# Optimization experiments

Hardware: AMD Instinct MI355X
Metric: run time of the kernel (lower is better)

The kernel has to match this reference:

```python
import jax, jax.numpy as jnp
import numpy as np

N = 8192       # patients (nodes)
E = 262144     # edges per graph (avg degree 32)
DF = 128       # dim_final
SLOPE = 0.25   # leaky_relu negative slope


def _spmm(rows, cols, vals, dense):
    # out[i] = sum_{e: rows[e]==i} vals[e] * dense[cols[e]]  == sparse_adj @ dense
    return jax.ops.segment_sum(vals[:, None] * dense[cols], rows, num_segments=N)


def _branch(x, rows, cols, vals, w1, b1, w2, b2):
    # GraphGCN: gc1 -> leaky_relu -> (dropout: identity in eval) -> gc2 -> leaky_relu
    h = _spmm(rows, cols, vals, x @ w1) + b1
    h = jax.nn.leaky_relu(h, negative_slope=SLOPE)
    h = _spmm(rows, cols, vals, h @ w2) + b2
    return jax.nn.leaky_relu(h, negative_slope=SLOPE)


def setup_inputs() -> dict:
    key = jax.random.key(0)
    ks = jax.random.split(key, 40)
    i = 0

    def xav(k, shape):
        std = (2.0 / (shape[0] + shape[1])) ** 0.5
        return std * jax.random.normal(k, shape, dtype=jnp.float32)

    inp = {}
    feat_dims = {"RNAseq": 4096, "dnam": 4096, "cn": 4096, "mic": 1024}
    for name, d in feat_dims.items():
        inp[name] = jax.random.normal(ks[i], (N, d), dtype=jnp.float32); i += 1
    for g in range(1, 5):
        inp[f"rows{g}"] = jax.random.randint(ks[i], (E,), 0, N, dtype=jnp.int32); i += 1
        inp[f"cols{g}"] = jax.random.randint(ks[i], (E,), 0, N, dtype=jnp.int32); i += 1
        inp[f"vals{g}"] = jax.random.uniform(ks[i], (E,), dtype=jnp.float32); i += 1
    # per-branch params: (in_dim, hid_dim); suffixes r=RNAseq, d=meth, c=CN, m=miRNA
    specs = {"r": (4096, 512), "d": (4096, 512), "c": (4096, 512), "m": (1024, 256)}
    for s, (din, dh) in specs.items():
        inp[f"w1_{s}"] = xav(ks[i], (din, dh)); i += 1
        inp[f"b1_{s}"] = jnp.zeros((dh,), jnp.float32)
        inp[f"w2_{s}"] = xav(ks[i], (dh, DF)); i += 1
        inp[f"b2_{s}"] = jnp.zeros((DF,), jnp.float32)
    return inp


def reference(RNAseq, dnam, cn, mic,
              rows1, cols1, vals1, rows2, cols2, vals2,
              rows3, cols3, vals3, rows4, cols4, vals4,
              w1_r, b1_r, w2_r, b2_r,
              w1_d, b1_d, w2_d, b2_d,
              w1_c, b1_c, w2_c, b2_c,
              w1_m, b1_m, w2_m, b2_m):
    x_r = _branch(RNAseq, rows1, cols1, vals1, w1_r, b1_r, w2_r, b2_r)
    x_d = _branch(dnam,   rows2, cols2, vals2, w1_d, b1_d, w2_d, b2_d)
    x_c = _branch(cn,     rows3, cols3, vals3, w1_c, b1_c, w2_c, b2_c)
    x_m = _branch(mic,    rows4, cols4, vals4, w1_m, b1_m, w2_m, b2_m)
    return (x_r + x_d + x_c + x_m) / 4.0
```

## Files before the change

kernel.cpp:

```cpp
#include <hip/hip_runtime.h>

#define N_NODES 8192
#define N_EDGES 262144
#define SLOPE 0.25f

typedef __attribute__((ext_vector_type(8))) short bf16x8;
typedef __attribute__((ext_vector_type(4))) float f32x4;

__device__ __forceinline__ float lrelu(float x) { return x >= 0.f ? x : SLOPE * x; }

__device__ __forceinline__ unsigned short bf16_rne(float x) {
    unsigned u = __float_as_uint(x);
    return (unsigned short)((u + 0x7FFFu + ((u >> 16) & 1u)) >> 16);
}
__device__ __forceinline__ float bf2f(unsigned short h) {
    return __uint_as_float(((unsigned)h) << 16);
}

#define GLDS16(g, l)                                                              \
    __builtin_amdgcn_global_load_lds((const __attribute__((address_space(1))) void*)(g), \
                                     (__attribute__((address_space(3))) void*)(l), 16, 0, 0)

struct RoundB { const float* src[4]; unsigned short* dst[4]; long long n4[4]; };

__global__ __launch_bounds__(256) void round_bf16(RoundB rb) {
    const int z = blockIdx.y;
    const long long i = (long long)blockIdx.x * 256 + threadIdx.x;
    if (i >= rb.n4[z]) return;
    const float4 a = reinterpret_cast<const float4*>(rb.src[z])[i];
    ushort4 h = {bf16_rne(a.x), bf16_rne(a.y), bf16_rne(a.z), bf16_rne(a.w)};
    reinterpret_cast<ushort4*>(rb.dst[z])[i] = h;
}

struct TransB { const float* W[4]; unsigned short* Th[4]; int K[4]; int N[4]; };

__global__ __launch_bounds__(256) void tsplit(TransB tb) {
    const int z = blockIdx.z;
    const int K = tb.K[z], N = tb.N[z];
    const int k0 = blockIdx.x * 32, n0 = blockIdx.y * 32;
    if (k0 >= K || n0 >= N) return;
    __shared__ float t[32][33];
    const int tx = threadIdx.x & 31, ty = threadIdx.x >> 5;
    const float* W = tb.W[z];
#pragma unroll
    for (int i = 0; i < 32; i += 8)
        t[ty + i][tx] = W[(size_t)(k0 + ty + i) * N + n0 + tx];
    __syncthreads();
#pragma unroll
    for (int i = 0; i < 32; i += 8) {
        const int n = ty + i;
        tb.Th[z][(size_t)(n0 + n) * K + k0 + tx] = bf16_rne(t[tx][n]);
    }
}

struct GemmB {
    const unsigned short* A[4];
    const unsigned short* Bh[4];
    unsigned short* C[4];
    int K[4];
    int NT[4];
};

template <int NF>
__global__ __launch_bounds__(256, 2) void gemm_bf16s(GemmB gb) {
    constexpr int BN = NF * 32;
    constexpr int BROWS = BN;
    constexpr int BGR_PER_THREAD = NF / 2;
    const int nwg = gridDim.x * gridDim.y * gridDim.z;
    int id = (blockIdx.z * gridDim.y + blockIdx.y) * gridDim.x + blockIdx.x;
    const int cpx = nwg >> 3;
    id = (id & 7) * cpx + (id >> 3);
    const int by = id % gridDim.y;
    const int rest = id / gridDim.y;
    const int bx = rest % gridDim.x;
    const int z = rest / gridDim.x;

    const int nt = gb.NT[z];
    if (by >= nt) return;
    const int K = gb.K[z];
    const int N = nt * BN;
    const unsigned short* __restrict__ A = gb.A[z];
    const unsigned short* __restrict__ Bh = gb.Bh[z];
    unsigned short* __restrict__ C = gb.C[z];

    __shared__ unsigned short As[3 * 128 * 32];
    __shared__ unsigned short Bs[3 * BROWS * 32];
    const int tid = threadIdx.x;
    const int w = tid >> 6, lane = tid & 63;
    const int wm = w >> 1, wn = w & 1;
    const int bm0 = bx * 128, bn0 = by * BN;

    auto stage = [&](int buf, int kt) {
        const int k0 = kt << 5;
#pragma unroll
        for (int i = 0; i < 2; ++i) {
            const int f = (w * 2 + i) * 64 + lane;
            const int row = f >> 2, s = f & 3;
            const int kg = s ^ ((row >> 1) & 3);
            GLDS16(A + (size_t)(bm0 + row) * K + k0 + kg * 8,
                   &As[buf * 4096 + (w * 2 + i) * 512]);
        }
#pragma unroll
        for (int i = 0; i < BGR_PER_THREAD; ++i) {
            const int f = (w * BGR_PER_THREAD + i) * 64 + lane;
            const int row = f >> 2, s = f & 3;
            const int kg = s ^ ((row >> 1) & 3);
            GLDS16(Bh + (size_t)(bn0 + row) * K + k0 + kg * 8,
                   &Bs[buf * (BROWS * 32) + (w * BGR_PER_THREAD + i) * 512]);
        }
    };

    f32x4 acc[4][NF];
#pragma unroll
    for (int mf = 0; mf < 4; ++mf)
#pragma unroll
        for (int nf = 0; nf < NF; ++nf) acc[mf][nf] = (f32x4){0.f, 0.f, 0.f, 0.f};

    const int nk = K >> 5;
    stage(0, 0);
    stage(1, 1);

    int c0 = 0, c1 = 1, c2 = 2;
    for (int t = 0; t < nk; ++t) {
        if (t + 2 < nk) {
            stage(c2, t + 2);
            if constexpr (NF == 8)
                asm volatile("s_waitcnt vmcnt(12)" ::: "memory");
            else
                asm volatile("s_waitcnt vmcnt(8)" ::: "memory");
        } else if (t + 1 < nk) {
            if constexpr (NF == 8)
                asm volatile("s_waitcnt vmcnt(6)" ::: "memory");
            else
                asm volatile("s_waitcnt vmcnt(4)" ::: "memory");
        } else {
            asm volatile("s_waitcnt vmcnt(0)" ::: "memory");
        }
        __builtin_amdgcn_s_barrier();
        __builtin_amdgcn_sched_barrier(0);

        const int kq = lane >> 4;
        bf16x8 a[4], b[NF];
#pragma unroll
        for (int mf = 0; mf < 4; ++mf) {
            const int r = wm * 64 + mf * 16 + (lane & 15);
            a[mf] = *reinterpret_cast<const bf16x8*>(
                &As[c0 * 4096 + r * 32 + ((kq ^ ((r >> 1) & 3)) << 3)]);
        }
#pragma unroll
        for (int nf = 0; nf < NF; ++nf) {
            const int r = wn * (NF * 16) + nf * 16 + (lane & 15);
            b[nf] = *reinterpret_cast<const bf16x8*>(
                &Bs[c0 * (BROWS * 32) + r * 32 + ((kq ^ ((r >> 1) & 3)) << 3)]);
        }
        __builtin_amdgcn_s_setprio(1);
#pragma unroll
        for (int mf = 0; mf < 4; ++mf)
#pragma unroll
            for (int nf = 0; nf < NF; ++nf)
                acc[mf][nf] = __builtin_amdgcn_mfma_f32_16x16x32_bf16(a[mf], b[nf], acc[mf][nf], 0, 0, 0);
        __builtin_amdgcn_s_setprio(0);

        __builtin_amdgcn_s_barrier();
        const int tmp = c0; c0 = c1; c1 = c2; c2 = tmp;
    }

    const int cr = (lane >> 4) * 4, cc = lane & 15;
#pragma unroll
    for (int mf = 0; mf < 4; ++mf)
#pragma unroll
        for (int nf = 0; nf < NF; ++nf)
#pragma unroll
            for (int j = 0; j < 4; ++j)
                C[(size_t)(bm0 + wm * 64 + mf * 16 + cr + j) * N + bn0 + wn * (NF * 16) + nf * 16 + cc] =
                    bf16_rne(acc[mf][nf][j]);
}

struct GraphPtrs {
    const int* r[4];
    const int* c[4];
    const float* v[4];
};

__global__ __launch_bounds__(256) void hist4(GraphPtrs p, int* __restrict__ cnt4) {
    const int g = blockIdx.y;
    const int e = blockIdx.x * 256 + threadIdx.x;
    atomicAdd(&cnt4[g * N_NODES + p.r[g][e]], 1);
}

__global__ __launch_bounds__(256) void scan4(const int* __restrict__ cnt4,
                                             int* __restrict__ rs4,
                                             int* __restrict__ cur4) {
    const int g = blockIdx.x;
    const int* cnt = cnt4 + g * N_NODES;
    int* row_start = rs4 + (size_t)g * (N_NODES + 1);
    int* cursor = cur4 + g * N_NODES;
    __shared__ int ssum[256];
    const int t = threadIdx.x;
    int local[32];
    int s = 0;
#pragma unroll
    for (int j = 0; j < 32; ++j) { local[j] = cnt[t * 32 + j]; s += local[j]; }
    ssum[t] = s;
    __syncthreads();
    for (int off = 1; off < 256; off <<= 1) {
        const int v = ssum[t];
        const int add = (t >= off) ? ssum[t - off] : 0;
        __syncthreads();
        ssum[t] = v + add;
        __syncthreads();
    }
    int run = (t == 0) ? 0 : ssum[t - 1];
#pragma unroll
    for (int j = 0; j < 32; ++j) {
        row_start[t * 32 + j] = run;
        cursor[t * 32 + j] = run;
        run += local[j];
    }
    if (t == 255) row_start[N_NODES] = run;
}

__global__ __launch_bounds__(256) void scatter4(GraphPtrs p, int* __restrict__ cur4,
                                                int* __restrict__ pcol4,
                                                float* __restrict__ pval4) {
    const int g = blockIdx.y;
    const int e = blockIdx.x * 256 + threadIdx.x;
    const int r = p.r[g][e];
    const int pos = atomicAdd(&cur4[g * N_NODES + r], 1);
    pcol4[(size_t)g * N_EDGES + pos] = p.c[g][e];
    pval4[(size_t)g * N_EDGES + pos] = p.v[g][e];
}

struct SpmmB {
    const int* rs[4];
    const int* pc[4];
    const float* pv[4];
    const unsigned short* Y[4];
    const float* bi[4];
    unsigned short* H[4];
};

template <int NC>
__global__ __launch_bounds__(256) void spmm_h1(SpmmB sb) {
    constexpr int PL = NC / 64;
    const int z = blockIdx.y;
    const int row = (blockIdx.x * 256 + threadIdx.x) >> 6;
    const int lane = threadIdx.x & 63;
    const int* rs = sb.rs[z];
    const int s = rs[row], e1 = rs[row + 1];
    const int* pc = sb.pc[z];
    const float* pv = sb.pv[z];
    const unsigned short* Y = sb.Y[z];
    const int base = lane * PL;

    float acc[PL];
#pragma unroll
    for (int j = 0; j < PL; ++j) acc[j] = 0.f;
    for (int e = s; e < e1; ++e) {
        const int c = pc[e];
        const float v = pv[e];
        const unsigned short* y = Y + (size_t)c * NC + base;
        if constexpr (PL == 8) {
            const bf16x8 raw = *reinterpret_cast<const bf16x8*>(y);
#pragma unroll
            for (int j = 0; j < 8; ++j)
                acc[j] = fmaf(v, bf2f((unsigned short)raw[j]), acc[j]);
        } else {
            const ushort4 raw = *reinterpret_cast<const ushort4*>(y);
            acc[0] = fmaf(v, bf2f(raw.x), acc[0]);
            acc[1] = fmaf(v, bf2f(raw.y), acc[1]);
            acc[2] = fmaf(v, bf2f(raw.z), acc[2]);
            acc[3] = fmaf(v, bf2f(raw.w), acc[3]);
        }
    }
    const float* bi = sb.bi[z];
    unsigned short* H = sb.H[z] + (size_t)row * NC + base;
    if constexpr (PL == 8) {
        bf16x8 vh;
#pragma unroll
        for (int j = 0; j < 8; ++j) vh[j] = (short)bf16_rne(lrelu(acc[j] + bi[base + j]));
        *reinterpret_cast<bf16x8*>(H) = vh;
    } else {
        ushort4 vh;
        vh.x = bf16_rne(lrelu(acc[0] + bi[base + 0]));
        vh.y = bf16_rne(lrelu(acc[1] + bi[base + 1]));
        vh.z = bf16_rne(lrelu(acc[2] + bi[base + 2]));
        vh.w = bf16_rne(lrelu(acc[3] + bi[base + 3]));
        *reinterpret_cast<ushort4*>(H) = vh;
    }
}

struct Out4 { const float* b2[4]; };

__global__ __launch_bounds__(256) void spmm_out4(const int* __restrict__ rs4,
                                                 const int* __restrict__ pc4,
                                                 const float* __restrict__ pv4,
                                                 const unsigned short* __restrict__ Y2all,
                                                 Out4 ob, float* __restrict__ out) {
    const int row = (blockIdx.x * 256 + threadIdx.x) >> 6;
    const int lane = threadIdx.x & 63;
    const int base = lane * 2;
    float r0 = 0.f, r1 = 0.f;
#pragma unroll
    for (int b = 0; b < 4; ++b) {
        const int* rs = rs4 + (size_t)b * (N_NODES + 1);
        const int s = rs[row], e1 = rs[row + 1];
        const int* pc = pc4 + (size_t)b * N_EDGES;
        const float* pv = pv4 + (size_t)b * N_EDGES;
        const unsigned short* Y = Y2all + (size_t)b * N_NODES * 128;
        float a0 = 0.f, a1 = 0.f;
        for (int e = s; e < e1; ++e) {
            const float v = pv[e];
            const unsigned u = *reinterpret_cast<const unsigned*>(Y + (size_t)pc[e] * 128 + base);
            a0 = fmaf(v, __uint_as_float(u << 16), a0);
            a1 = fmaf(v, __uint_as_float(u & 0xFFFF0000u), a1);
        }
        const float* bi = ob.b2[b];
        r0 += lrelu(a0 + bi[base]);
        r1 += lrelu(a1 + bi[base + 1]);
    }
    *reinterpret_cast<float2*>(out + (size_t)row * 128 + base) =
        make_float2(0.25f * r0, 0.25f * r1);
}

__global__ __launch_bounds__(256) void spmm_out1(const int* __restrict__ rs,
                                                 const int* __restrict__ pc,
                                                 const float* __restrict__ pv,
                                                 const unsigned short* __restrict__ Y,
                                                 const float* __restrict__ bias,
                                                 float* __restrict__ out, int first) {
    const int row = (blockIdx.x * 256 + threadIdx.x) >> 6;
    const int lane = threadIdx.x & 63;
    const int base = lane * 2;
    const int s = rs[row], e1 = rs[row + 1];
    float a0 = 0.f, a1 = 0.f;
    for (int e = s; e < e1; ++e) {
        const float v = pv[e];
        const unsigned u = *reinterpret_cast<const unsigned*>(Y + (size_t)pc[e] * 128 + base);
        a0 = fmaf(v, __uint_as_float(u << 16), a0);
        a1 = fmaf(v, __uint_as_float(u & 0xFFFF0000u), a1);
    }
    float r0 = 0.25f * lrelu(a0 + bias[base]);
    float r1 = 0.25f * lrelu(a1 + bias[base + 1]);
    float* o = out + (size_t)row * 128 + base;
    if (!first) {
        const float2 p = *reinterpret_cast<const float2*>(o);
        r0 += p.x;
        r1 += p.y;
    }
    *reinterpret_cast<float2*>(o) = make_float2(r0, r1);
}

extern "C" void kernel_launch(void* const* d_in, const int* in_sizes, int n_in,
                              void* d_out, int out_size, void* d_ws, size_t ws_size,
                              hipStream_t stream) {
    const float* X[4] = {(const float*)d_in[0], (const float*)d_in[1],
                         (const float*)d_in[2], (const float*)d_in[3]};
    GraphPtrs gp;
    for (int b = 0; b < 4; ++b) {
        gp.r[b] = (const int*)d_in[4 + 3 * b];
        gp.c[b] = (const int*)d_in[5 + 3 * b];
        gp.v[b] = (const float*)d_in[6 + 3 * b];
    }
    const float *w1[4], *b1[4], *w2[4], *b2[4];
    for (int b = 0; b < 4; ++b) {
        w1[b] = (const float*)d_in[16 + 4 * b + 0];
        b1[b] = (const float*)d_in[16 + 4 * b + 1];
        w2[b] = (const float*)d_in[16 + 4 * b + 2];
        b2[b] = (const float*)d_in[16 + 4 * b + 3];
    }
    const int din[4] = {4096, 4096, 4096, 1024};
    const int dh[4] = {512, 512, 512, 256};
    float* out = (float*)d_out;

    char* wsc = (char*)d_ws;
    size_t off = 0;
    auto carve = [&](size_t bytes) {
        void* p = wsc + off;
        off += (bytes + 255) & ~(size_t)255;
        return p;
    };
    int* cnt4 = (int*)carve((size_t)4 * N_NODES * 4);
    int* rs4 = (int*)carve((size_t)4 * (N_NODES + 1) * 4);
    int* cur4 = (int*)carve((size_t)4 * N_NODES * 4);
    int* pcol4 = (int*)carve((size_t)4 * N_EDGES * 4);
    float* pval4 = (float*)carve((size_t)4 * N_EDGES * 4);

    size_t tier1_base = off;
    unsigned short *Xbf[4], *W1h[4], *W2h[4], *Y1[4], *H1[4];
    for (int b = 0; b < 4; ++b) Xbf[b] = (unsigned short*)carve((size_t)N_NODES * din[b] * 2);
    for (int b = 0; b < 4; ++b) W1h[b] = (unsigned short*)carve((size_t)dh[b] * din[b] * 2);
    for (int b = 0; b < 4; ++b) W2h[b] = (unsigned short*)carve((size_t)128 * dh[b] * 2);
    for (int b = 0; b < 4; ++b) Y1[b] = (unsigned short*)carve((size_t)N_NODES * dh[b] * 2);
    for (int b = 0; b < 4; ++b) H1[b] = (unsigned short*)carve((size_t)N_NODES * dh[b] * 2);
    unsigned short* Y2all = (unsigned short*)carve((size_t)4 * N_NODES * 128 * 2);
    const bool tier1 = (off <= ws_size);
    unsigned short* Y2s[4];
    if (tier1) {
        for (int b = 0; b < 4; ++b) Y2s[b] = Y2all + (size_t)b * N_NODES * 128;
    } else {
        off = tier1_base;
        unsigned short* xb = (unsigned short*)carve((size_t)N_NODES * 4096 * 2);
        unsigned short* w1h = (unsigned short*)carve((size_t)512 * 4096 * 2);
        unsigned short* w2h = (unsigned short*)carve((size_t)128 * 512 * 2);
        unsigned short* y1 = (unsigned short*)carve((size_t)N_NODES * 512 * 2);
        unsigned short* h1 = (unsigned short*)carve((size_t)N_NODES * 512 * 2);
        unsigned short* y2 = (unsigned short*)carve((size_t)N_NODES * 128 * 2);
        for (int b = 0; b < 4; ++b) {
            Xbf[b] = xb; W1h[b] = w1h; W2h[b] = w2h;
            Y1[b] = y1; H1[b] = h1; Y2s[b] = y2;
        }
    }

    hipMemsetAsync(cnt4, 0, (size_t)4 * N_NODES * sizeof(int), stream);
    {
        dim3 g(N_EDGES / 256, 4);
        hist4<<<g, 256, 0, stream>>>(gp, cnt4);
        scan4<<<4, 256, 0, stream>>>(cnt4, rs4, cur4);
        scatter4<<<g, 256, 0, stream>>>(gp, cur4, pcol4, pval4);
    }

    if (tier1) {
        RoundB rb;
        for (int b = 0; b < 4; ++b) {
            rb.src[b] = X[b];
            rb.dst[b] = Xbf[b];
            rb.n4[b] = (long long)N_NODES * din[b] / 4;
        }
        round_bf16<<<dim3(32768, 4), 256, 0, stream>>>(rb);

        TransB t1;
        for (int b = 0; b < 4; ++b) {
            t1.W[b] = w1[b]; t1.Th[b] = W1h[b];
            t1.K[b] = din[b]; t1.N[b] = dh[b];
        }
        tsplit<<<dim3(128, 16, 4), 256, 0, stream>>>(t1);

        GemmB g1;
        for (int b = 0; b < 4; ++b) {
            g1.A[b] = Xbf[b]; g1.Bh[b] = W1h[b];
            g1.C[b] = Y1[b]; g1.K[b] = din[b]; g1.NT[b] = dh[b] / 256;
        }
        gemm_bf16s<8><<<dim3(64, 2, 4), 256, 0, stream>>>(g1);

        SpmmB s1;
        for (int b = 0; b < 4; ++b) {
            s1.rs[b] = rs4 + (size_t)b * (N_NODES + 1);
            s1.pc[b] = pcol4 + (size_t)b * N_EDGES;
            s1.pv[b] = pval4 + (size_t)b * N_EDGES;
            s1.Y[b] = Y1[b]; s1.bi[b] = b1[b]; s1.H[b] = H1[b];
        }
        spmm_h1<512><<<dim3(N_NODES / 4, 3), 256, 0, stream>>>(s1);
        SpmmB s1m = s1;
        s1m.rs[0] = s1.rs[3]; s1m.pc[0] = s1.pc[3]; s1m.pv[0] = s1.pv[3];
        s1m.Y[0] = s1.Y[3]; s1m.bi[0] = s1.bi[3]; s1m.H[0] = s1.H[3];
        spmm_h1<256><<<dim3(N_NODES / 4, 1), 256, 0, stream>>>(s1m);

        TransB t2;
        for (int b = 0; b < 4; ++b) {
            t2.W[b] = w2[b]; t2.Th[b] = W2h[b];
            t2.K[b] = dh[b]; t2.N[b] = 128;
        }
        tsplit<<<dim3(16, 4, 4), 256, 0, stream>>>(t2);

        GemmB g2;
        for (int b = 0; b < 4; ++b) {
            g2.A[b] = H1[b]; g2.Bh[b] = W2h[b];
            g2.C[b] = Y2s[b]; g2.K[b] = dh[b]; g2.NT[b] = 1;
        }
        gemm_bf16s<4><<<dim3(64, 1, 4), 256, 0, stream>>>(g2);

        Out4 ob;
        for (int b = 0; b < 4; ++b) ob.b2[b] = b2[b];
        spmm_out4<<<N_NODES / 4, 256, 0, stream>>>(rs4, pcol4, pval4, Y2all, ob, out);
    } else {
        for (int b = 0; b < 4; ++b) {
            RoundB rb;
            rb.src[0] = X[b]; rb.dst[0] = Xbf[b];
            rb.n4[0] = (long long)N_NODES * din[b] / 4;
            round_bf16<<<dim3((unsigned)(rb.n4[0] / 256), 1), 256, 0, stream>>>(rb);
            TransB t1;
            t1.W[0] = w1[b]; t1.Th[0] = W1h[b];
            t1.K[0] = din[b]; t1.N[0] = dh[b];
            tsplit<<<dim3(din[b] / 32, dh[b] / 32, 1), 256, 0, stream>>>(t1);
            GemmB g1;
            g1.A[0] = Xbf[b]; g1.Bh[0] = W1h[b];
            g1.C[0] = Y1[b]; g1.K[0] = din[b]; g1.NT[0] = dh[b] / 256;
            gemm_bf16s<8><<<dim3(64, dh[b] / 256, 1), 256, 0, stream>>>(g1);
            SpmmB s1;
            s1.rs[0] = rs4 + (size_t)b * (N_NODES + 1);
            s1.pc[0] = pcol4 + (size_t)b * N_EDGES;
            s1.pv[0] = pval4 + (size_t)b * N_EDGES;
            s1.Y[0] = Y1[b]; s1.bi[0] = b1[b]; s1.H[0] = H1[b];
            if (dh[b] == 512)
                spmm_h1<512><<<dim3(N_NODES / 4, 1), 256, 0, stream>>>(s1);
            else
                spmm_h1<256><<<dim3(N_NODES / 4, 1), 256, 0, stream>>>(s1);
            TransB t2;
            t2.W[0] = w2[b]; t2.Th[0] = W2h[b];
            t2.K[0] = dh[b]; t2.N[0] = 128;
            tsplit<<<dim3(dh[b] / 32, 4, 1), 256, 0, stream>>>(t2);
            GemmB g2;
            g2.A[0] = H1[b]; g2.Bh[0] = W2h[b];
            g2.C[0] = Y2s[b]; g2.K[0] = dh[b]; g2.NT[0] = 1;
            gemm_bf16s<4><<<dim3(64, 1, 1), 256, 0, stream>>>(g2);
            spmm_out1<<<N_NODES / 4, 256, 0, stream>>>(
                rs4 + (size_t)b * (N_NODES + 1), pcol4 + (size_t)b * N_EDGES,
                pval4 + (size_t)b * N_EDGES, Y2s[b], b2[b], out, b == 0);
        }
    }
}
```

Before: 621.3 us.

## Fuse fp32-to-bf16 input conversion into GEMM A loading and pack edge records

Removes the separate rounding kernel by having the first GEMM load fp32 activations through registers, convert them to bf16 and write them into LDS with the same swizzle, using a double register set across the three-stage pipeline. Column index and value are packed into one 64-bit record per edge so the SpMM kernels do a single load per edge. This removes a full extra read and write pass over the large feature matrices. In exchange the GEMM reads twice as many bytes for A and gains register pressure and an extra VGPR-to-LDS write path.

```diff
diff --git a/kernel.cpp b/kernel.cpp
--- a/kernel.cpp
+++ b/kernel.cpp
@@ -16,21 +16,18 @@
 __device__ __forceinline__ float bf2f(unsigned short h) {
     return __uint_as_float(((unsigned)h) << 16);
 }
+__device__ __forceinline__ bf16x8 pack8(const float4& a, const float4& b) {
+    bf16x8 r;
+    r[0] = (short)bf16_rne(a.x); r[1] = (short)bf16_rne(a.y);
+    r[2] = (short)bf16_rne(a.z); r[3] = (short)bf16_rne(a.w);
+    r[4] = (short)bf16_rne(b.x); r[5] = (short)bf16_rne(b.y);
+    r[6] = (short)bf16_rne(b.z); r[7] = (short)bf16_rne(b.w);
+    return r;
+}
 
 #define GLDS16(g, l)                                                              \
     __builtin_amdgcn_global_load_lds((const __attribute__((address_space(1))) void*)(g), \
                                      (__attribute__((address_space(3))) void*)(l), 16, 0, 0)
-
-struct RoundB { const float* src[4]; unsigned short* dst[4]; long long n4[4]; };
-
-__global__ __launch_bounds__(256) void round_bf16(RoundB rb) {
-    const int z = blockIdx.y;
-    const long long i = (long long)blockIdx.x * 256 + threadIdx.x;
-    if (i >= rb.n4[z]) return;
-    const float4 a = reinterpret_cast<const float4*>(rb.src[z])[i];
-    ushort4 h = {bf16_rne(a.x), bf16_rne(a.y), bf16_rne(a.z), bf16_rne(a.w)};
-    reinterpret_cast<ushort4*>(rb.dst[z])[i] = h;
-}
 
 struct TransB { const float* W[4]; unsigned short* Th[4]; int K[4]; int N[4]; };
 
@@ -54,18 +51,16 @@
 }
 
 struct GemmB {
-    const unsigned short* A[4];
+    const void* A[4];
     const unsigned short* Bh[4];
     unsigned short* C[4];
     int K[4];
     int NT[4];
 };
 
-template <int NF>
+template <int NF, int AF32>
 __global__ __launch_bounds__(256, 2) void gemm_bf16s(GemmB gb) {
-    constexpr int BN = NF * 32;
-    constexpr int BROWS = BN;
-    constexpr int BGR_PER_THREAD = NF / 2;
+    constexpr int BGR = NF / 2;
     const int nwg = gridDim.x * gridDim.y * gridDim.z;
     int id = (blockIdx.z * gridDim.y + blockIdx.y) * gridDim.x + blockIdx.x;
     const int cpx = nwg >> 3;
@@ -78,37 +73,59 @@
     const int nt = gb.NT[z];
     if (by >= nt) return;
     const int K = gb.K[z];
-    const int N = nt * BN;
-    const unsigned short* __restrict__ A = gb.A[z];
+    const int N = nt * (NF * 32);
+    const float* __restrict__ Af = (const float*)gb.A[z];
+    const unsigned short* __restrict__ Ab = (const unsigned short*)gb.A[z];
     const unsigned short* __restrict__ Bh = gb.Bh[z];
     unsigned short* __restrict__ C = gb.C[z];
 
-    __shared__ unsigned short As[3 * 128 * 32];
-    __shared__ unsigned short Bs[3 * BROWS * 32];
+    __shared__ unsigned short As[3 * 4096];
+    __shared__ unsigned short Bs[3 * NF * 1024];
     const int tid = threadIdx.x;
     const int w = tid >> 6, lane = tid & 63;
     const int wm = w >> 1, wn = w & 1;
-    const int bm0 = bx * 128, bn0 = by * BN;
-
-    auto stage = [&](int buf, int kt) {
+    const int bm0 = bx * 128, bn0 = by * (NF * 32);
+
+    auto stageB = [&](int buf, int kt) {
+        const int k0 = kt << 5;
+#pragma unroll
+        for (int i = 0; i < BGR; ++i) {
+            const int f = (w * BGR + i) * 64 + lane;
+            const int row = f >> 2, s = f & 3;
+            const int kg = s ^ ((row >> 1) & 3);
+            GLDS16(Bh + (size_t)(bn0 + row) * K + k0 + kg * 8,
+                   &Bs[buf * (NF * 1024) + (w * BGR + i) * 512]);
+        }
+    };
+    auto stageAglds = [&](int buf, int kt) {
         const int k0 = kt << 5;
 #pragma unroll
         for (int i = 0; i < 2; ++i) {
             const int f = (w * 2 + i) * 64 + lane;
             const int row = f >> 2, s = f & 3;
             const int kg = s ^ ((row >> 1) & 3);
-            GLDS16(A + (size_t)(bm0 + row) * K + k0 + kg * 8,
+            GLDS16(Ab + (size_t)(bm0 + row) * K + k0 + kg * 8,
                    &As[buf * 4096 + (w * 2 + i) * 512]);
         }
-#pragma unroll
-        for (int i = 0; i < BGR_PER_THREAD; ++i) {
-            const int f = (w * BGR_PER_THREAD + i) * 64 + lane;
+    };
+    auto issueA = [&](float4 (&ar)[2][2], int kt) {
+        const int k0 = kt << 5;
+#pragma unroll
+        for (int i = 0; i < 2; ++i) {
+            const int f = i * 256 + tid;
             const int row = f >> 2, s = f & 3;
             const int kg = s ^ ((row >> 1) & 3);
-            GLDS16(Bh + (size_t)(bn0 + row) * K + k0 + kg * 8,
-                   &Bs[buf * (BROWS * 32) + (w * BGR_PER_THREAD + i) * 512]);
+            const float* src = Af + (size_t)(bm0 + row) * K + k0 + kg * 8;
+            ar[i][0] = *reinterpret_cast<const float4*>(src);
+            ar[i][1] = *reinterpret_cast<const float4*>(src + 4);
         }
     };
+    auto writeA = [&](float4 (&ar)[2][2], int buf) {
+#pragma unroll
+        for (int i = 0; i < 2; ++i)
+            *reinterpret_cast<bf16x8*>(&As[buf * 4096 + (i * 256 + tid) * 8]) =
+                pack8(ar[i][0], ar[i][1]);
+    };
 
     f32x4 acc[4][NF];
 #pragma unroll
@@ -117,27 +134,43 @@
         for (int nf = 0; nf < NF; ++nf) acc[mf][nf] = (f32x4){0.f, 0.f, 0.f, 0.f};
 
     const int nk = K >> 5;
-    stage(0, 0);
-    stage(1, 1);
-
-    int c0 = 0, c1 = 1, c2 = 2;
-    for (int t = 0; t < nk; ++t) {
+    float4 aE[2][2], aO[2][2];
+
+    if constexpr (AF32) {
+        issueA(aE, 0); stageB(0, 0);
+        issueA(aO, 1); stageB(1, 1);
+        asm volatile("s_waitcnt vmcnt(12)" ::: "memory");
+        writeA(aE, 0);
+        asm volatile("s_waitcnt lgkmcnt(0)" ::: "memory");
+    } else {
+        stageAglds(0, 0); stageB(0, 0);
+        stageAglds(1, 1); stageB(1, 1);
+    }
+
+    auto body = [&](int t, float4 (&iset)[2][2], float4 (&wset)[2][2]) {
+        const int cb = t % 3;
         if (t + 2 < nk) {
-            stage(c2, t + 2);
-            if constexpr (NF == 8)
-                asm volatile("s_waitcnt vmcnt(12)" ::: "memory");
-            else
-                asm volatile("s_waitcnt vmcnt(8)" ::: "memory");
+            if constexpr (AF32) issueA(iset, t + 2);
+            else stageAglds((t + 2) % 3, t + 2);
+            stageB((t + 2) % 3, t + 2);
+            if constexpr (AF32) asm volatile("s_waitcnt vmcnt(16)" ::: "memory");
+            else asm volatile("s_waitcnt vmcnt(8)" ::: "memory");
         } else if (t + 1 < nk) {
-            if constexpr (NF == 8)
-                asm volatile("s_waitcnt vmcnt(6)" ::: "memory");
-            else
-                asm volatile("s_waitcnt vmcnt(4)" ::: "memory");
+            if constexpr (AF32) asm volatile("s_waitcnt vmcnt(8)" ::: "memory");
+            else asm volatile("s_waitcnt vmcnt(4)" ::: "memory");
         } else {
             asm volatile("s_waitcnt vmcnt(0)" ::: "memory");
         }
         __builtin_amdgcn_s_barrier();
         __builtin_amdgcn_sched_barrier(0);
+
+        if constexpr (AF32) {
+            if (t + 1 < nk) {
+                if (t + 2 < nk) asm volatile("s_waitcnt vmcnt(12)" ::: "memory");
+                else asm volatile("s_waitcnt vmcnt(4)" ::: "memory");
+                writeA(wset, (t + 1) % 3);
+            }
+        }
 
         const int kq = lane >> 4;
         bf16x8 a[4], b[NF];
@@ -145,13 +178,13 @@
         for (int mf = 0; mf < 4; ++mf) {
             const int r = wm * 64 + mf * 16 + (lane & 15);
             a[mf] = *reinterpret_cast<const bf16x8*>(
-                &As[c0 * 4096 + r * 32 + ((kq ^ ((r >> 1) & 3)) << 3)]);
+                &As[cb * 4096 + r * 32 + ((kq ^ ((r >> 1) & 3)) << 3)]);
         }
 #pragma unroll
         for (int nf = 0; nf < NF; ++nf) {
             const int r = wn * (NF * 16) + nf * 16 + (lane & 15);
             b[nf] = *reinterpret_cast<const bf16x8*>(
-                &Bs[c0 * (BROWS * 32) + r * 32 + ((kq ^ ((r >> 1) & 3)) << 3)]);
+                &Bs[cb * (NF * 1024) + r * 32 + ((kq ^ ((r >> 1) & 3)) << 3)]);
         }
         __builtin_amdgcn_s_setprio(1);
 #pragma unroll
@@ -161,8 +194,13 @@
                 acc[mf][nf] = __builtin_amdgcn_mfma_f32_16x16x32_bf16(a[mf], b[nf], acc[mf][nf], 0, 0, 0);
         __builtin_amdgcn_s_setprio(0);
 
+        asm volatile("s_waitcnt lgkmcnt(0)" ::: "memory");
         __builtin_amdgcn_s_barrier();
-        const int tmp = c0; c0 = c1; c1 = c2; c2 = tmp;
+    };
+
+    for (int t = 0; t < nk; t += 2) {
+        body(t, aE, aO);
+        body(t + 1, aO, aE);
     }
 
     const int cr = (lane >> 4) * 4, cc = lane & 15;
@@ -221,20 +259,19 @@
 }
 
 __global__ __launch_bounds__(256) void scatter4(GraphPtrs p, int* __restrict__ cur4,
-                                                int* __restrict__ pcol4,
-                                                float* __restrict__ pval4) {
+                                                unsigned long long* __restrict__ pe4) {
     const int g = blockIdx.y;
     const int e = blockIdx.x * 256 + threadIdx.x;
     const int r = p.r[g][e];
     const int pos = atomicAdd(&cur4[g * N_NODES + r], 1);
-    pcol4[(size_t)g * N_EDGES + pos] = p.c[g][e];
-    pval4[(size_t)g * N_EDGES + pos] = p.v[g][e];
+    pe4[(size_t)g * N_EDGES + pos] =
+        (unsigned long long)(unsigned)p.c[g][e] |
+        ((unsigned long long)__float_as_uint(p.v[g][e]) << 32);
 }
 
 struct SpmmB {
     const int* rs[4];
-    const int* pc[4];
-    const float* pv[4];
+    const unsigned long long* pe[4];
     const unsigned short* Y[4];
     const float* bi[4];
     unsigned short* H[4];
@@ -248,8 +285,7 @@
     const int lane = threadIdx.x & 63;
     const int* rs = sb.rs[z];
     const int s = rs[row], e1 = rs[row + 1];
-    const int* pc = sb.pc[z];
-    const float* pv = sb.pv[z];
+    const unsigned long long* pe = sb.pe[z];
     const unsigned short* Y = sb.Y[z];
     const int base = lane * PL;
 
@@ -257,8 +293,9 @@
 #pragma unroll
     for (int j = 0; j < PL; ++j) acc[j] = 0.f;
     for (int e = s; e < e1; ++e) {
-        const int c = pc[e];
-        const float v = pv[e];
+        const unsigned long long ev = pe[e];
+        const int c = (int)(unsigned)ev;
+        const float v = __uint_as_float((unsigned)(ev >> 32));
         const unsigned short* y = Y + (size_t)c * NC + base;
         if constexpr (PL == 8) {
             const bf16x8 raw = *reinterpret_cast<const bf16x8*>(y);
@@ -293,8 +330,7 @@
 struct Out4 { const float* b2[4]; };
 
 __global__ __launch_bounds__(256) void spmm_out4(const int* __restrict__ rs4,
-                                                 const int* __restrict__ pc4,
-                                                 const float* __restrict__ pv4,
+                                                 const unsigned long long* __restrict__ pe4,
                                                  const unsigned short* __restrict__ Y2all,
                                                  Out4 ob, float* __restrict__ out) {
     const int row = (blockIdx.x * 256 + threadIdx.x) >> 6;
@@ -305,13 +341,14 @@
     for (int b = 0; b < 4; ++b) {
         const int* rs = rs4 + (size_t)b * (N_NODES + 1);
         const int s = rs[row], e1 = rs[row + 1];
-        const int* pc = pc4 + (size_t)b * N_EDGES;
-        const float* pv = pv4 + (size_t)b * N_EDGES;
+        const unsigned long long* pe = pe4 + (size_t)b * N_EDGES;
         const unsigned short* Y = Y2all + (size_t)b * N_NODES * 128;
         float a0 = 0.f, a1 = 0.f;
         for (int e = s; e < e1; ++e) {
-            const float v = pv[e];
-            const unsigned u = *reinterpret_cast<const unsigned*>(Y + (size_t)pc[e] * 128 + base);
+            const unsigned long long ev = pe[e];
+            const float v = __uint_as_float((unsigned)(ev >> 32));
+            const unsigned u = *reinterpret_cast<const unsigned*>(
+                Y + (size_t)(unsigned)ev * 128 + base);
             a0 = fmaf(v, __uint_as_float(u << 16), a0);
             a1 = fmaf(v, __uint_as_float(u & 0xFFFF0000u), a1);
         }
@@ -324,8 +361,7 @@
 }
 
 __global__ __launch_bounds__(256) void spmm_out1(const int* __restrict__ rs,
-                                                 const int* __restrict__ pc,
-                                                 const float* __restrict__ pv,
+                                                 const unsigned long long* __restrict__ pe,
                                                  const unsigned short* __restrict__ Y,
                                                  const float* __restrict__ bias,
                                                  float* __restrict__ out, int first) {
@@ -335,8 +371,10 @@
     const int s = rs[row], e1 = rs[row + 1];
     float a0 = 0.f, a1 = 0.f;
     for (int e = s; e < e1; ++e) {
-        const float v = pv[e];
-        const unsigned u = *reinterpret_cast<const unsigned*>(Y + (size_t)pc[e] * 128 + base);
+        const unsigned long long ev = pe[e];
+        const float v = __uint_as_float((unsigned)(ev >> 32));
+        const unsigned u = *reinterpret_cast<const unsigned*>(
+            Y + (size_t)(unsigned)ev * 128 + base);
         a0 = fmaf(v, __uint_as_float(u << 16), a0);
         a1 = fmaf(v, __uint_as_float(u & 0xFFFF0000u), a1);
     }
@@ -383,12 +421,10 @@
     int* cnt4 = (int*)carve((size_t)4 * N_NODES * 4);
     int* rs4 = (int*)carve((size_t)4 * (N_NODES + 1) * 4);
     int* cur4 = (int*)carve((size_t)4 * N_NODES * 4);
-    int* pcol4 = (int*)carve((size_t)4 * N_EDGES * 4);
-    float* pval4 = (float*)carve((size_t)4 * N_EDGES * 4);
+    unsigned long long* pe4 = (unsigned long long*)carve((size_t)4 * N_EDGES * 8);
 
     size_t tier1_base = off;
-    unsigned short *Xbf[4], *W1h[4], *W2h[4], *Y1[4], *H1[4];
-    for (int b = 0; b < 4; ++b) Xbf[b] = (unsigned short*)carve((size_t)N_NODES * din[b] * 2);
+    unsigned short *W1h[4], *W2h[4], *Y1[4], *H1[4];
     for (int b = 0; b < 4; ++b) W1h[b] = (unsigned short*)carve((size_t)dh[b] * din[b] * 2);
     for (int b = 0; b < 4; ++b) W2h[b] = (unsigned short*)carve((size_t)128 * dh[b] * 2);
     for (int b = 0; b < 4; ++b) Y1[b] = (unsigned short*)carve((size_t)N_NODES * dh[b] * 2);
@@ -400,14 +436,13 @@
         for (int b = 0; b < 4; ++b) Y2s[b] = Y2all + (size_t)b * N_NODES * 128;
     } else {
         off = tier1_base;
-        unsigned short* xb = (unsigned short*)carve((size_t)N_NODES * 4096 * 2);
         unsigned short* w1h = (unsigned short*)carve((size_t)512 * 4096 * 2);
         unsigned short* w2h = (unsigned short*)carve((size_t)128 * 512 * 2);
         unsigned short* y1 = (unsigned short*)carve((size_t)N_NODES * 512 * 2);
         unsigned short* h1 = (unsigned short*)carve((size_t)N_NODES * 512 * 2);
         unsigned short* y2 = (unsigned short*)carve((size_t)N_NODES * 128 * 2);
         for (int b = 0; b < 4; ++b) {
-            Xbf[b] = xb; W1h[b] = w1h; W2h[b] = w2h;
+            W1h[b] = w1h; W2h[b] = w2h;
             Y1[b] = y1; H1[b] = h1; Y2s[b] = y2;
         }
     }
@@ -417,18 +452,10 @@
         dim3 g(N_EDGES / 256, 4);
         hist4<<<g, 256, 0, stream>>>(gp, cnt4);
         scan4<<<4, 256, 0, stream>>>(cnt4, rs4, cur4);
-        scatter4<<<g, 256, 0, stream>>>(gp, cur4, pcol4, pval4);
+        scatter4<<<g, 256, 0, stream>>>(gp, cur4, pe4);
     }
 
     if (tier1) {
-        RoundB rb;
-        for (int b = 0; b < 4; ++b) {
-            rb.src[b] = X[b];
-            rb.dst[b] = Xbf[b];
-            rb.n4[b] = (long long)N_NODES * din[b] / 4;
-        }
-        round_bf16<<<dim3(32768, 4), 256, 0, stream>>>(rb);
-
         TransB t1;
         for (int b = 0; b < 4; ++b) {
             t1.W[b] = w1[b]; t1.Th[b] = W1h[b];
@@ -438,21 +465,20 @@
 
         GemmB g1;
         for (int b = 0; b < 4; ++b) {
-            g1.A[b] = Xbf[b]; g1.Bh[b] = W1h[b];
+            g1.A[b] = X[b]; g1.Bh[b] = W1h[b];
             g1.C[b] = Y1[b]; g1.K[b] = din[b]; g1.NT[b] = dh[b] / 256;
         }
-        gemm_bf16s<8><<<dim3(64, 2, 4), 256, 0, stream>>>(g1);
+        gemm_bf16s<8, 1><<<dim3(64, 2, 4), 256, 0, stream>>>(g1);
 
         SpmmB s1;
         for (int b = 0; b < 4; ++b) {
             s1.rs[b] = rs4 + (size_t)b * (N_NODES + 1);
-            s1.pc[b] = pcol4 + (size_t)b * N_EDGES;
-            s1.pv[b] = pval4 + (size_t)b * N_EDGES;
+            s1.pe[b] = pe4 + (size_t)b * N_EDGES;
             s1.Y[b] = Y1[b]; s1.bi[b] = b1[b]; s1.H[b] = H1[b];
         }
         spmm_h1<512><<<dim3(N_NODES / 4, 3), 256, 0, stream>>>(s1);
         SpmmB s1m = s1;
-        s1m.rs[0] = s1.rs[3]; s1m.pc[0] = s1.pc[3]; s1m.pv[0] = s1.pv[3];
+        s1m.rs[0] = s1.rs[3]; s1m.pe[0] = s1.pe[3];
         s1m.Y[0] = s1.Y[3]; s1m.bi[0] = s1.bi[3]; s1m.H[0] = s1.H[3];
         spmm_h1<256><<<dim3(N_NODES / 4, 1), 256, 0, stream>>>(s1m);
 
@@ -468,29 +494,24 @@
             g2.A[b] = H1[b]; g2.Bh[b] = W2h[b];
             g2.C[b] = Y2s[b]; g2.K[b] = dh[b]; g2.NT[b] = 1;
         }
-        gemm_bf16s<4><<<dim3(64, 1, 4), 256, 0, stream>>>(g2);
+        gemm_bf16s<4, 0><<<dim3(64, 1, 4), 256, 0, stream>>>(g2);
 
         Out4 ob;
         for (int b = 0; b < 4; ++b) ob.b2[b] = b2[b];
-        spmm_out4<<<N_NODES / 4, 256, 0, stream>>>(rs4, pcol4, pval4, Y2all, ob, out);
+        spmm_out4<<<N_NODES / 4, 256, 0, stream>>>(rs4, pe4, Y2all, ob, out);
     } else {
         for (int b = 0; b < 4; ++b) {
-            RoundB rb;
-            rb.src[0] = X[b]; rb.dst[0] = Xbf[b];
-            rb.n4[0] = (long long)N_NODES * din[b] / 4;
-            round_bf16<<<dim3((unsigned)(rb.n4[0] / 256), 1), 256, 0, stream>>>(rb);
             TransB t1;
             t1.W[0] = w1[b]; t1.Th[0] = W1h[b];
             t1.K[0] = din[b]; t1.N[0] = dh[b];
             tsplit<<<dim3(din[b] / 32, dh[b] / 32, 1), 256, 0, stream>>>(t1);
             GemmB g1;
-            g1.A[0] = Xbf[b]; g1.Bh[0] = W1h[b];
+            g1.A[0] = X[b]; g1.Bh[0] = W1h[b];
             g1.C[0] = Y1[b]; g1.K[0] = din[b]; g1.NT[0] = dh[b] / 256;
-            gemm_bf16s<8><<<dim3(64, dh[b] / 256, 1), 256, 0, stream>>>(g1);
+            gemm_bf16s<8, 1><<<dim3(64, dh[b] / 256, 1), 256, 0, stream>>>(g1);
             SpmmB s1;
             s1.rs[0] = rs4 + (size_t)b * (N_NODES + 1);
-            s1.pc[0] = pcol4 + (size_t)b * N_EDGES;
-            s1.pv[0] = pval4 + (size_t)b * N_EDGES;
+            s1.pe[0] = pe4 + (size_t)b * N_EDGES;
             s1.Y[0] = Y1[b]; s1.bi[0] = b1[b]; s1.H[0] = H1[b];
             if (dh[b] == 512)
                 spmm_h1<512><<<dim3(N_NODES / 4, 1), 256, 0, stream>>>(s1);
@@ -503,10 +524,10 @@
             GemmB g2;
             g2.A[0] = H1[b]; g2.Bh[0] = W2h[b];
             g2.C[0] = Y2s[b]; g2.K[0] = dh[b]; g2.NT[0] = 1;
-            gemm_bf16s<4><<<dim3(64, 1, 1), 256, 0, stream>>>(g2);
+            gemm_bf16s<4, 0><<<dim3(64, 1, 1), 256, 0, stream>>>(g2);
             spmm_out1<<<N_NODES / 4, 256, 0, stream>>>(
-                rs4 + (size_t)b * (N_NODES + 1), pcol4 + (size_t)b * N_EDGES,
-                pval4 + (size_t)b * N_EDGES, Y2s[b], b2[b], out, b == 0);
-        }
-    }
-}
+                rs4 + (size_t)b * (N_NODES + 1), pe4 + (size_t)b * N_EDGES,
+                Y2s[b], b2[b], out, b == 0);
+        }
+    }
+}
```

Result: faster. 533.1 us (-14.2%).
